# Optimization experiments

Hardware: AMD Instinct MI355X
Metric: run time of the kernel (lower is better)

## Reference

```python
import jax, jax.numpy as jnp
import numpy as np
from jax import lax

B, C1, C2, CM, H, W, K = 8, 256, 256, 128, 80, 80, 3
N = K * K
PAD = 1
EPS = 1e-5  # nn.BatchNorm2d default eps


def _bn(x, g, b, m, v):
    # eval-mode BatchNorm2d, NCHW
    inv = g / jnp.sqrt(v + EPS)
    return x * inv[None, :, None, None] + (b - m * inv)[None, :, None, None]


def _conv1x1(x, w):  # w: [O, I]
    return jnp.einsum('bihw,oi->bohw', x, w)


def _conv3x3(x, w, b):  # w: [O, I, 3, 3]
    y = lax.conv_general_dilated(x, w, window_strides=(1, 1),
                                 padding=((PAD, PAD), (PAD, PAD)),
                                 dimension_numbers=('NCHW', 'OIHW', 'NCHW'))
    return y + b[None, :, None, None]


def _deform_conv2d(x, offset, mask, w, bias):
    # DCNv2 (torchvision deform_conv2d semantics), stride=1, pad=1, k=3.
    # x: [B,C,H,W]; offset: [B,2N,H,W] pairs (dy,dx) per kernel tap (row-major);
    # mask: [B,N,H,W]; w: [O,C,3,3]
    Bx, C, Hx, Wx = x.shape
    ky, kx = jnp.meshgrid(jnp.arange(K), jnp.arange(K), indexing='ij')
    ky = ky.reshape(N).astype(x.dtype)
    kx = kx.reshape(N).astype(x.dtype)
    off = offset.reshape(Bx, N, 2, Hx, Wx)
    # sampling positions [B,N,H,W]
    py = (jnp.arange(Hx, dtype=x.dtype)[None, None, :, None] - PAD
          + ky[None, :, None, None] + off[:, :, 0])
    px = (jnp.arange(Wx, dtype=x.dtype)[None, None, None, :] - PAD
          + kx[None, :, None, None] + off[:, :, 1])

    y0 = jnp.floor(py)
    x0 = jnp.floor(px)
    wy1 = py - y0  # frac weights
    wx1 = px - x0
    x_flat = x.reshape(Bx, C, Hx * Wx)

    def corner(yi, xi, wgt):
        valid = (yi >= 0) & (yi < Hx) & (xi >= 0) & (xi < Wx)
        yc = jnp.clip(yi, 0, Hx - 1).astype(jnp.int32)
        xc = jnp.clip(xi, 0, Wx - 1).astype(jnp.int32)
        idx = (yc * Wx + xc).reshape(Bx, 1, N * Hx * Wx)
        g = jnp.take_along_axis(x_flat, idx, axis=2).reshape(Bx, C, N, Hx, Wx)
        return g * (wgt * valid.astype(x.dtype))[:, None]

    sampled = (corner(y0, x0, (1 - wy1) * (1 - wx1))
               + corner(y0, x0 + 1, (1 - wy1) * wx1)
               + corner(y0 + 1, x0, wy1 * (1 - wx1))
               + corner(y0 + 1, x0 + 1, wy1 * wx1))
    sampled = sampled * mask[:, None]  # modulated (v2)
    out = jnp.einsum('bcnhw,ocn->bohw', sampled, w.reshape(w.shape[0], C, N))
    return out + bias[None, :, None, None]


def setup_inputs() -> dict:
    key = jax.random.key(0)
    ks = jax.random.split(key, 20)
    f32 = jnp.float32
    d = {}
    d['x'] = jax.random.normal(ks[0], (B, C1, H, W), dtype=f32)
    # cv1: 1x1 conv (no bias) + BN
    d['cv1_w'] = jax.random.normal(ks[1], (CM, C1), dtype=f32) * (1.0 / np.sqrt(C1))
    d['bn1_g'] = jax.random.uniform(ks[2], (CM,), dtype=f32, minval=0.5, maxval=1.5)
    d['bn1_b'] = jax.random.normal(ks[3], (CM,), dtype=f32) * 0.1
    d['bn1_m'] = jax.random.normal(ks[4], (CM,), dtype=f32) * 0.1
    d['bn1_v'] = jax.random.uniform(ks[5], (CM,), dtype=f32, minval=0.5, maxval=1.5)
    # offset conv: predicts 3*N channels (2N offsets + N mask logits)
    d['off_w'] = jax.random.normal(ks[6], (3 * N, CM, K, K), dtype=f32) * 0.01
    d['off_b'] = jax.random.normal(ks[7], (3 * N,), dtype=f32) * 0.1
    # deformable conv main weight/bias
    d['dcn_w'] = jax.random.normal(ks[8], (CM, CM, K, K), dtype=f32) * np.sqrt(2.0 / (CM * N))
    d['dcn_b'] = jnp.zeros((CM,), dtype=f32)
    d['bn2_g'] = jax.random.uniform(ks[9], (CM,), dtype=f32, minval=0.5, maxval=1.5)
    d['bn2_b'] = jax.random.normal(ks[10], (CM,), dtype=f32) * 0.1
    d['bn2_m'] = jax.random.normal(ks[11], (CM,), dtype=f32) * 0.1
    d['bn2_v'] = jax.random.uniform(ks[12], (CM,), dtype=f32, minval=0.5, maxval=1.5)
    # cv3: 1x1 conv + BN
    d['cv3_w'] = jax.random.normal(ks[13], (C2, CM), dtype=f32) * (1.0 / np.sqrt(CM))
    d['bn3_g'] = jax.random.uniform(ks[14], (C2,), dtype=f32, minval=0.5, maxval=1.5)
    d['bn3_b'] = jax.random.normal(ks[15], (C2,), dtype=f32) * 0.1
    d['bn3_m'] = jax.random.normal(ks[16], (C2,), dtype=f32) * 0.1
    d['bn3_v'] = jax.random.uniform(ks[17], (C2,), dtype=f32, minval=0.5, maxval=1.5)
    return d


def reference(x, cv1_w, bn1_g, bn1_b, bn1_m, bn1_v,
              off_w, off_b, dcn_w, dcn_b,
              bn2_g, bn2_b, bn2_m, bn2_v,
              cv3_w, bn3_g, bn3_b, bn3_m, bn3_v):
    y = jax.nn.silu(_bn(_conv1x1(x, cv1_w), bn1_g, bn1_b, bn1_m, bn1_v))
    pred = _conv3x3(y, off_w, off_b)          # [B,3N,H,W]
    offset = pred[:, :2 * N]
    mask = jax.nn.sigmoid(pred[:, 2 * N:])
    y = _deform_conv2d(y, offset, mask, dcn_w, dcn_b)
    y = jax.nn.silu(_bn(y, bn2_g, bn2_b, bn2_m, bn2_v))
    y = jax.nn.silu(_bn(_conv1x1(y, cv3_w), bn3_g, bn3_b, bn3_m, bn3_v))
    return x + y  # shortcut: c1 == c2
```

## Files before the change

### kernel.cpp

```cpp
#include <hip/hip_runtime.h>
#include <math.h>

#define HWX   6400
#define WID   80
#define HGT   80
#define CMID  128
#define CIN   256
#define COUT  256

#define WS_PRED 0
#define WS_BN   1382400
#define WS_Y2   1383424
#define WS_Z2   4660224
#define WS_WPK  7937024
#define WS_WPO  8010752
#define WS_WP1  8029184
#define WS_WP3  8045568

typedef float floatx16 __attribute__((ext_vector_type(16)));
typedef short shortx8  __attribute__((ext_vector_type(8)));
typedef float floatx2  __attribute__((ext_vector_type(2)));

union U8 { uint32_t u[4]; shortx8 s; };

__device__ __forceinline__ float silu_f(float t){ return t / (1.f + __expf(-t)); }
__device__ __forceinline__ uint32_t f2bf(float f){
    uint32_t u = __float_as_uint(f);
    return (u + 0x7fffu + ((u >> 16) & 1u)) >> 16;
}
__device__ __forceinline__ floatx2 up2(uint32_t u){
    floatx2 r; r.x = __uint_as_float(u << 16); r.y = __uint_as_float(u & 0xffff0000u); return r;
}
__device__ __forceinline__ uint32_t pk2(floatx2 v){
    return __builtin_amdgcn_perm(__float_as_uint(v.y) + 0x8000u,
                                 __float_as_uint(v.x) + 0x8000u, 0x07060302u);
}
__device__ __forceinline__ uint32_t pk2f(float a, float b){ floatx2 v; v.x=a; v.y=b; return pk2(v); }

__global__ __launch_bounds__(256) void k0_prep(
    const float* __restrict__ dcn_w, const float* __restrict__ off_w,
    const float* __restrict__ cv1_w, const float* __restrict__ cv3_w,
    const float* __restrict__ g1, const float* __restrict__ b1, const float* __restrict__ m1, const float* __restrict__ v1,
    const float* __restrict__ g2, const float* __restrict__ b2, const float* __restrict__ m2, const float* __restrict__ v2,
    const float* __restrict__ dcn_b,
    const float* __restrict__ g3, const float* __restrict__ b3, const float* __restrict__ m3, const float* __restrict__ v3,
    uint32_t* __restrict__ wpk, uint32_t* __restrict__ wpo,
    uint32_t* __restrict__ wp1, uint32_t* __restrict__ wp3, float* __restrict__ bnw)
{
    int i = blockIdx.x * 256 + threadIdx.x;
    if (i < 4*9*8*256) {
        int j = i & 3, lane = (i >> 2) & 63, s = (i >> 8) & 7;
        int r2 = i >> 11; int tap = r2 % 9, g = r2 / 9;
        int oc = g*32 + (lane & 31);
        int c  = s*16 + ((lane >> 5) << 3) + 2*j;
        wpk[i] = f2bf(dcn_w[(oc*128 + c)*9 + tap]) | (f2bf(dcn_w[(oc*128 + c + 1)*9 + tap]) << 16);
    }
    if (i < 9*8*256) {
        int j = i & 3, lane = (i >> 2) & 63, s = (i >> 8) & 7, tap = i >> 11;
        int oc = lane & 31;
        int c  = s*16 + ((lane >> 5) << 3) + 2*j;
        float lo = (oc < 27) ? off_w[(oc*128 + c)*9 + tap] : 0.f;
        float hi = (oc < 27) ? off_w[(oc*128 + c + 1)*9 + tap] : 0.f;
        wpo[i] = f2bf(lo) | (f2bf(hi) << 16);
    }
    if (i < 4*16*256) {
        int j = i & 3, lane = (i >> 2) & 63, s = (i >> 8) & 15, g = i >> 12;
        int oc = g*32 + (lane & 31);
        int c  = s*16 + ((lane >> 5) << 3) + 2*j;
        wp1[i] = f2bf(cv1_w[oc*256 + c]) | (f2bf(cv1_w[oc*256 + c + 1]) << 16);
    }
    if (i < 8*8*256) {
        int j = i & 3, lane = (i >> 2) & 63, s = (i >> 8) & 7, g = i >> 11;
        int oc = g*32 + (lane & 31);
        int c  = s*16 + ((lane >> 5) << 3) + 2*j;
        wp3[i] = f2bf(cv3_w[oc*128 + c]) | (f2bf(cv3_w[oc*128 + c + 1]) << 16);
    }
    if (i < 128) {
        float inv = g1[i] * rsqrtf(v1[i] + 1e-5f);
        bnw[i] = inv; bnw[128+i] = b1[i] - m1[i]*inv;
    } else if (i < 256) {
        int j = i - 128;
        float inv = g2[j] * rsqrtf(v2[j] + 1e-5f);
        bnw[256+j] = inv; bnw[384+j] = b2[j] - m2[j]*inv + inv*dcn_b[j];
    } else if (i < 512) {
        int j = i - 256;
        float inv = g3[j] * rsqrtf(v3[j] + 1e-5f);
        bnw[512+j] = inv; bnw[768+j] = b3[j] - m3[j]*inv;
    }
}

#define K1PAD 68
__global__ __launch_bounds__(256) void k1_cv1(
    const float* __restrict__ x, const uint32_t* __restrict__ wp1,
    const float* __restrict__ bn, uint32_t* __restrict__ y2)
{
    __shared__ __align__(16) uint32_t L[64*66];
    int blk = blockIdx.x;
    int b = blk / 100, pix0 = (blk % 100) * 64;
    int t = threadIdx.x;
    int lane = t & 63, w = t >> 6;
    int pixl = lane & 31, bhalf = lane >> 5;
    floatx16 acc0 = {}, acc1 = {};
    const float* xb = x + (size_t)b*CIN*HWX + pix0;
    const uint32_t* wpg = wp1 + (size_t)(w*16)*256 + lane*4;

    int r2 = t >> 4, c4 = (t & 15) * 4;
    for (int kk = 0; kk < 256; kk += 32) {
        float4 a0 = *(const float4*)(xb + (size_t)(kk + 2*r2)*HWX + c4);
        float4 a1 = *(const float4*)(xb + (size_t)(kk + 2*r2 + 1)*HWX + c4);
        uint4 q;
        q.x = pk2f(a0.x, a1.x);
        q.y = pk2f(a0.y, a1.y);
        q.z = pk2f(a0.z, a1.z);
        q.w = pk2f(a0.w, a1.w);
        __syncthreads();
        *(uint4*)&L[r2*K1PAD + c4] = q;
        __syncthreads();
        #pragma unroll
        for (int sl = 0; sl < 2; sl++) {
            int s = (kk >> 4) + sl;
            U8 a, b0, b1;
            const uint32_t* as = wpg + s*256;
            a.u[0]=as[0]; a.u[1]=as[1]; a.u[2]=as[2]; a.u[3]=as[3];
            int row = sl*8 + bhalf*4;
            #pragma unroll
            for (int j = 0; j < 4; j++) b0.u[j] = L[(row+j)*K1PAD + pixl];
            #pragma unroll
            for (int j = 0; j < 4; j++) b1.u[j] = L[(row+j)*K1PAD + 32 + pixl];
            acc0 = __builtin_amdgcn_mfma_f32_32x32x16_bf16(a.s, b0.s, acc0, 0, 0, 0);
            acc1 = __builtin_amdgcn_mfma_f32_32x32x16_bf16(a.s, b1.s, acc1, 0, 0, 0);
        }
    }
    __syncthreads();
    #pragma unroll
    for (int r = 0; r < 16; r += 2) {
        int oc = w*32 + (r & 3) + 8*(r >> 2) + 4*bhalf;
        float s0 = bn[oc],   be0 = bn[128+oc];
        float s1 = bn[oc+1], be1 = bn[128+oc+1];
        uint32_t d0 = pk2f(silu_f(acc0[r]*s0+be0), silu_f(acc0[r+1]*s1+be1));
        uint32_t d1 = pk2f(silu_f(acc1[r]*s0+be0), silu_f(acc1[r+1]*s1+be1));
        int oc2 = oc >> 1;
        L[pixl*66 + oc2]        = d0;
        L[(32+pixl)*66 + oc2]   = d1;
    }
    __syncthreads();
    uint32_t* y2b = y2 + (size_t)b*HWX*64 + (size_t)pix0*64;
    int q2 = t & 31, p0 = t >> 5;
    #pragma unroll
    for (int pp = 0; pp < 8; pp++) {
        int pix = p0 + pp*8;
        uint2 v = make_uint2(L[pix*66 + q2*2], L[pix*66 + q2*2 + 1]);
        *(uint2*)(y2b + (size_t)pix*64 + q2*2) = v;
    }
}

__global__ __launch_bounds__(256) void k2_off(
    const uint32_t* __restrict__ y2, const uint32_t* __restrict__ wpo,
    const float* __restrict__ ob, float* __restrict__ pred)
{
    int blk = blockIdx.x;
    int b = blk / 50, pix0 = (blk % 50) * 128;
    int t = threadIdx.x;
    int lane = t & 63, w = t >> 6;
    int pixl = lane & 31, half = lane >> 5;
    int p = pix0 + w*32 + pixl;
    int h = p / WID, xw = p % WID;
    const uint32_t* yb = y2 + (size_t)b*HWX*64;
    floatx16 acc = {};

    for (int tap = 0; tap < 9; tap++) {
        int dy = tap/3 - 1, dx = tap%3 - 1;
        int gh = h + dy, gx = xw + dx;
        bool valid = (gh >= 0) && (gh < HGT) && (gx >= 0) && (gx < WID);
        const uint32_t* pp = yb + (size_t)(gh*WID + gx)*64 + half*4;
        const uint32_t* ap = wpo + (size_t)(tap*8)*256 + lane*4;
        #pragma unroll
        for (int s = 0; s < 8; s++) {
            U8 a, bf;
            const uint32_t* as = ap + s*256;
            a.u[0]=as[0]; a.u[1]=as[1]; a.u[2]=as[2]; a.u[3]=as[3];
            if (valid) {
                uint4 q = *(const uint4*)(pp + s*8);
                bf.u[0]=q.x; bf.u[1]=q.y; bf.u[2]=q.z; bf.u[3]=q.w;
            } else {
                bf.u[0]=0u; bf.u[1]=0u; bf.u[2]=0u; bf.u[3]=0u;
            }
            acc = __builtin_amdgcn_mfma_f32_32x32x16_bf16(a.s, bf.s, acc, 0, 0, 0);
        }
    }
    float* pb = pred + (size_t)b*27*HWX;
    #pragma unroll
    for (int r = 0; r < 16; r++) {
        int oc = (r & 3) + 8*(r >> 2) + 4*half;
        if (oc < 27) {
            float v = acc[r] + ob[oc];
            if (oc >= 18) v = 1.f/(1.f+__expf(-v));
            pb[oc*HWX + p] = v;
        }
    }
}

#define S2R 68
__global__ __launch_bounds__(256) void k3_dcn(
    const uint32_t* __restrict__ y2, const float* __restrict__ pred,
    const uint32_t* __restrict__ wpk, const float* __restrict__ bn, uint32_t* __restrict__ z2)
{
    __shared__ __align__(16) uint32_t S2[2][32*S2R];
    __shared__ __align__(16) int   sidx9[9*32*4];
    __shared__ __align__(16) float swgt9[9*32*4];
    int blk = blockIdx.x;
    int b = blk / 200, pix0 = (blk % 200) * 32;
    int t = threadIdx.x;
    int lane = t & 63, w = t >> 6;
    int pixl = lane & 31, bhalf = lane >> 5;
    const float* pb = pred + (size_t)b*27*HWX;
    const uint32_t* yb = y2 + (size_t)b*HWX*64;
    floatx16 acc = {};
    int c4 = lane & 31, pixoff = lane >> 5;

    for (int it = t; it < 288; it += 256) {
        int tap = it >> 5, px = it & 31;
        int pix = pix0 + px;
        int h = pix / WID, wq = pix % WID;
        float dy = pb[(2*tap)*HWX + pix];
        float dx = pb[(2*tap+1)*HWX + pix];
        float mk = pb[(18+tap)*HWX + pix];
        float pyf = (float)(h - 1 + tap/3) + dy;
        float pxf = (float)(wq - 1 + tap%3) + dx;
        float y0f = floorf(pyf), x0f = floorf(pxf);
        float wy1 = pyf - y0f, wx1 = pxf - x0f;
        int iy0 = (int)y0f, ix0 = (int)x0f;
        int iy1 = iy0 + 1,  ix1 = ix0 + 1;
        float vy0 = (iy0 >= 0 && iy0 < HGT) ? 1.f : 0.f;
        float vy1 = (iy1 >= 0 && iy1 < HGT) ? 1.f : 0.f;
        float vx0 = (ix0 >= 0 && ix0 < WID) ? 1.f : 0.f;
        float vx1 = (ix1 >= 0 && ix1 < WID) ? 1.f : 0.f;
        int cy0 = min(max(iy0,0),HGT-1), cy1 = min(max(iy1,0),HGT-1);
        int cx0 = min(max(ix0,0),WID-1), cx1 = min(max(ix1,0),WID-1);
        int base = (tap*32 + px)*4;
        sidx9[base+0] = cy0*WID+cx0; sidx9[base+1] = cy0*WID+cx1;
        sidx9[base+2] = cy1*WID+cx0; sidx9[base+3] = cy1*WID+cx1;
        swgt9[base+0] = (1.f-wy1)*(1.f-wx1)*mk*vy0*vx0;
        swgt9[base+1] = (1.f-wy1)*wx1*mk*vy0*vx1;
        swgt9[base+2] = wy1*(1.f-wx1)*mk*vy1*vx0;
        swgt9[base+3] = wy1*wx1*mk*vy1*vx1;
    }
    __syncthreads();

    uint2  u[4][4];
    float4 W[4];
    uint2  samp[4];

    #pragma unroll
    for (int p = 0; p < 4; p++) {
        int pix = w*8 + p*2 + pixoff;
        int base = (0*32 + pix)*4;
        int4 si = *(const int4*)&sidx9[base];
        W[p] = *(const float4*)&swgt9[base];
        u[p][0] = *(const uint2*)(yb + (size_t)si.x*64 + c4*2);
        u[p][1] = *(const uint2*)(yb + (size_t)si.y*64 + c4*2);
        u[p][2] = *(const uint2*)(yb + (size_t)si.z*64 + c4*2);
        u[p][3] = *(const uint2*)(yb + (size_t)si.w*64 + c4*2);
    }
    #pragma unroll
    for (int p = 0; p < 4; p++) {
        floatx2 W0, W1, W2, W3;
        W0.x = W0.y = W[p].x; W1.x = W1.y = W[p].y;
        W2.x = W2.y = W[p].z; W3.x = W3.y = W[p].w;
        floatx2 aX = up2(u[p][0].x) * W0;
        aX = __builtin_elementwise_fma(up2(u[p][1].x), W1, aX);
        aX = __builtin_elementwise_fma(up2(u[p][2].x), W2, aX);
        aX = __builtin_elementwise_fma(up2(u[p][3].x), W3, aX);
        floatx2 aY = up2(u[p][0].y) * W0;
        aY = __builtin_elementwise_fma(up2(u[p][1].y), W1, aY);
        aY = __builtin_elementwise_fma(up2(u[p][2].y), W2, aY);
        aY = __builtin_elementwise_fma(up2(u[p][3].y), W3, aY);
        samp[p].x = pk2(aX); samp[p].y = pk2(aY);
    }

    #pragma unroll
    for (int tap = 0; tap < 9; tap++) {
        uint32_t* S = &S2[tap & 1][0];
        #pragma unroll
        for (int p = 0; p < 4; p++) {
            int pix = w*8 + p*2 + pixoff;
            *(uint2*)&S[pix*S2R + c4*2] = samp[p];
        }
        __syncthreads();
        if (tap < 8) {
            #pragma unroll
            for (int p = 0; p < 4; p++) {
                int pix = w*8 + p*2 + pixoff;
                int base = ((tap+1)*32 + pix)*4;
                int4 si = *(const int4*)&sidx9[base];
                W[p] = *(const float4*)&swgt9[base];
                u[p][0] = *(const uint2*)(yb + (size_t)si.x*64 + c4*2);
                u[p][1] = *(const uint2*)(yb + (size_t)si.y*64 + c4*2);
                u[p][2] = *(const uint2*)(yb + (size_t)si.z*64 + c4*2);
                u[p][3] = *(const uint2*)(yb + (size_t)si.w*64 + c4*2);
            }
        }
        const uint32_t* wp = wpk + (size_t)((w*9 + tap)*8)*256 + lane*4;
        #pragma unroll
        for (int s = 0; s < 8; s++) {
            U8 a, bf;
            const uint32_t* wps = wp + s*256;
            a.u[0] = wps[0]; a.u[1] = wps[1]; a.u[2] = wps[2]; a.u[3] = wps[3];
            uint4 q = *(const uint4*)&S[pixl*S2R + s*8 + bhalf*4];
            bf.u[0]=q.x; bf.u[1]=q.y; bf.u[2]=q.z; bf.u[3]=q.w;
            acc = __builtin_amdgcn_mfma_f32_32x32x16_bf16(a.s, bf.s, acc, 0, 0, 0);
        }
        if (tap < 8) {
            #pragma unroll
            for (int p = 0; p < 4; p++) {
                floatx2 W0, W1, W2, W3;
                W0.x = W0.y = W[p].x; W1.x = W1.y = W[p].y;
                W2.x = W2.y = W[p].z; W3.x = W3.y = W[p].w;
                floatx2 aX = up2(u[p][0].x) * W0;
                aX = __builtin_elementwise_fma(up2(u[p][1].x), W1, aX);
                aX = __builtin_elementwise_fma(up2(u[p][2].x), W2, aX);
                aX = __builtin_elementwise_fma(up2(u[p][3].x), W3, aX);
                floatx2 aY = up2(u[p][0].y) * W0;
                aY = __builtin_elementwise_fma(up2(u[p][1].y), W1, aY);
                aY = __builtin_elementwise_fma(up2(u[p][2].y), W2, aY);
                aY = __builtin_elementwise_fma(up2(u[p][3].y), W3, aY);
                samp[p].x = pk2(aX); samp[p].y = pk2(aY);
            }
        }
    }
    uint32_t* SE = &S2[1][0];
    #pragma unroll
    for (int r = 0; r < 16; r += 2) {
        int oc = w*32 + (r & 3) + 8*(r >> 2) + 4*bhalf;
        float s0 = bn[256+oc],   be0 = bn[384+oc];
        float s1 = bn[256+oc+1], be1 = bn[384+oc+1];
        SE[pixl*S2R + (oc >> 1)] = pk2f(silu_f(acc[r]*s0+be0), silu_f(acc[r+1]*s1+be1));
    }
    __syncthreads();
    uint32_t* z2b = z2 + (size_t)b*HWX*64 + (size_t)pix0*64;
    int q2 = t & 31, p0 = t >> 5;
    #pragma unroll
    for (int pp = 0; pp < 4; pp++) {
        int pix = p0 + pp*8;
        uint2 v = *(const uint2*)&SE[pix*S2R + q2*2];
        *(uint2*)(z2b + (size_t)pix*64 + q2*2) = v;
    }
}

__global__ __launch_bounds__(256) void k4_cv3(
    const uint32_t* __restrict__ z2, const uint32_t* __restrict__ wp3,
    const float* __restrict__ bn, const float* __restrict__ x, float* __restrict__ out)
{
    int blk = blockIdx.x;
    int half = blk & 1, blk2 = blk >> 1;
    int b = blk2 / 100, pix0 = (blk2 % 100) * 64;
    int t = threadIdx.x;
    int lane = t & 63, w = t >> 6;
    int pixl = lane & 31, bhalf = lane >> 5;
    int g = half*4 + w;
    floatx16 acc0 = {}, acc1 = {};
    const uint32_t* zb = z2 + (size_t)b*HWX*64 + (size_t)pix0*64;
    const uint32_t* wpg = wp3 + (size_t)(g*8)*256 + lane*4;

    #pragma unroll
    for (int s = 0; s < 8; s++) {
        U8 a, b0, b1;
        const uint32_t* as = wpg + s*256;
        a.u[0]=as[0]; a.u[1]=as[1]; a.u[2]=as[2]; a.u[3]=as[3];
        uint4 q0 = *(const uint4*)(zb + (size_t)pixl*64 + s*8 + bhalf*4);
        uint4 q1 = *(const uint4*)(zb + (size_t)(32+pixl)*64 + s*8 + bhalf*4);
        b0.u[0]=q0.x; b0.u[1]=q0.y; b0.u[2]=q0.z; b0.u[3]=q0.w;
        b1.u[0]=q1.x; b1.u[1]=q1.y; b1.u[2]=q1.z; b1.u[3]=q1.w;
        acc0 = __builtin_amdgcn_mfma_f32_32x32x16_bf16(a.s, b0.s, acc0, 0, 0, 0);
        acc1 = __builtin_amdgcn_mfma_f32_32x32x16_bf16(a.s, b1.s, acc1, 0, 0, 0);
    }
    const float* xb = x + (size_t)b*COUT*HWX + pix0;
    float* ob = out + (size_t)b*COUT*HWX + pix0;
    #pragma unroll
    for (int r = 0; r < 16; r++) {
        int oc = g*32 + (r & 3) + 8*(r >> 2) + 4*bhalf;
        float sc = bn[512+oc], be = bn[768+oc];
        float v0 = silu_f(acc0[r]*sc+be) + xb[(size_t)oc*HWX + pixl];
        float v1 = silu_f(acc1[r]*sc+be) + xb[(size_t)oc*HWX + 32 + pixl];
        ob[(size_t)oc*HWX + pixl]      = v0;
        ob[(size_t)oc*HWX + 32 + pixl] = v1;
    }
}

extern "C" void kernel_launch(void* const* d_in, const int* in_sizes, int n_in,
                              void* d_out, int out_size, void* d_ws, size_t ws_size,
                              hipStream_t stream) {
    const float* x     = (const float*)d_in[0];
    const float* cv1_w = (const float*)d_in[1];
    const float* bn1_g = (const float*)d_in[2];
    const float* bn1_b = (const float*)d_in[3];
    const float* bn1_m = (const float*)d_in[4];
    const float* bn1_v = (const float*)d_in[5];
    const float* off_w = (const float*)d_in[6];
    const float* off_b = (const float*)d_in[7];
    const float* dcn_w = (const float*)d_in[8];
    const float* dcn_b = (const float*)d_in[9];
    const float* bn2_g = (const float*)d_in[10];
    const float* bn2_b = (const float*)d_in[11];
    const float* bn2_m = (const float*)d_in[12];
    const float* bn2_v = (const float*)d_in[13];
    const float* cv3_w = (const float*)d_in[14];
    const float* bn3_g = (const float*)d_in[15];
    const float* bn3_b = (const float*)d_in[16];
    const float* bn3_m = (const float*)d_in[17];
    const float* bn3_v = (const float*)d_in[18];

    float* ws   = (float*)d_ws;
    float*    PRED = ws + WS_PRED;
    float*    BN   = ws + WS_BN;
    uint32_t* Y2   = (uint32_t*)(ws + WS_Y2);
    uint32_t* Z2   = (uint32_t*)(ws + WS_Z2);
    uint32_t* WPK  = (uint32_t*)(ws + WS_WPK);
    uint32_t* WPO  = (uint32_t*)(ws + WS_WPO);
    uint32_t* WP1  = (uint32_t*)(ws + WS_WP1);
    uint32_t* WP3  = (uint32_t*)(ws + WS_WP3);

    hipLaunchKernelGGL(k0_prep, dim3(288), dim3(256), 0, stream,
        dcn_w, off_w, cv1_w, cv3_w,
        bn1_g, bn1_b, bn1_m, bn1_v,
        bn2_g, bn2_b, bn2_m, bn2_v, dcn_b,
        bn3_g, bn3_b, bn3_m, bn3_v, WPK, WPO, WP1, WP3, BN);
    hipLaunchKernelGGL(k1_cv1, dim3(800), dim3(256), 0, stream, x, WP1, BN, Y2);
    hipLaunchKernelGGL(k2_off, dim3(400), dim3(256), 0, stream, Y2, WPO, off_b, PRED);
    hipLaunchKernelGGL(k3_dcn, dim3(1600), dim3(256), 0, stream, Y2, PRED, WPK, BN, Z2);
    hipLaunchKernelGGL(k4_cv3, dim3(1600), dim3(256), 0, stream, Z2, WP3, BN, x, (float*)d_out);
}
```

Baseline: 238.6 us.

## Fuse offset/mask conv into deformable conv kernel, dropping pred buffer

Removes the separate offset-prediction kernel and computes the 3x3 offset/mask conv inside the DCN kernel for each 32-pixel tile. The taps are split across the 4 waves and the partial sums are reduced through shared memory reused from the S2 buffer. This avoids a kernel launch and the global write and read of the 27-channel pred tensor. In exchange it adds MFMA work and global neighbour loads to every DCN block, with only 32 pixels per tile, plus an extra shared-memory reduction and two barriers.

```diff
diff --git a/kernel.cpp b/kernel.cpp
--- a/kernel.cpp
+++ b/kernel.cpp
@@ -8,14 +8,13 @@
 #define CIN   256
 #define COUT  256
 
-#define WS_PRED 0
-#define WS_BN   1382400
-#define WS_Y2   1383424
-#define WS_Z2   4660224
-#define WS_WPK  7937024
-#define WS_WPO  8010752
-#define WS_WP1  8029184
-#define WS_WP3  8045568
+#define WS_BN   0
+#define WS_Y2   1024
+#define WS_Z2   3277824
+#define WS_WPK  6554624
+#define WS_WPO  6628352
+#define WS_WP1  6646784
+#define WS_WP3  6663168
 
 typedef float floatx16 __attribute__((ext_vector_type(16)));
 typedef short shortx8  __attribute__((ext_vector_type(8)));
@@ -154,55 +153,10 @@
     }
 }
 
-__global__ __launch_bounds__(256) void k2_off(
-    const uint32_t* __restrict__ y2, const uint32_t* __restrict__ wpo,
-    const float* __restrict__ ob, float* __restrict__ pred)
-{
-    int blk = blockIdx.x;
-    int b = blk / 50, pix0 = (blk % 50) * 128;
-    int t = threadIdx.x;
-    int lane = t & 63, w = t >> 6;
-    int pixl = lane & 31, half = lane >> 5;
-    int p = pix0 + w*32 + pixl;
-    int h = p / WID, xw = p % WID;
-    const uint32_t* yb = y2 + (size_t)b*HWX*64;
-    floatx16 acc = {};
-
-    for (int tap = 0; tap < 9; tap++) {
-        int dy = tap/3 - 1, dx = tap%3 - 1;
-        int gh = h + dy, gx = xw + dx;
-        bool valid = (gh >= 0) && (gh < HGT) && (gx >= 0) && (gx < WID);
-        const uint32_t* pp = yb + (size_t)(gh*WID + gx)*64 + half*4;
-        const uint32_t* ap = wpo + (size_t)(tap*8)*256 + lane*4;
-        #pragma unroll
-        for (int s = 0; s < 8; s++) {
-            U8 a, bf;
-            const uint32_t* as = ap + s*256;
-            a.u[0]=as[0]; a.u[1]=as[1]; a.u[2]=as[2]; a.u[3]=as[3];
-            if (valid) {
-                uint4 q = *(const uint4*)(pp + s*8);
-                bf.u[0]=q.x; bf.u[1]=q.y; bf.u[2]=q.z; bf.u[3]=q.w;
-            } else {
-                bf.u[0]=0u; bf.u[1]=0u; bf.u[2]=0u; bf.u[3]=0u;
-            }
-            acc = __builtin_amdgcn_mfma_f32_32x32x16_bf16(a.s, bf.s, acc, 0, 0, 0);
-        }
-    }
-    float* pb = pred + (size_t)b*27*HWX;
-    #pragma unroll
-    for (int r = 0; r < 16; r++) {
-        int oc = (r & 3) + 8*(r >> 2) + 4*half;
-        if (oc < 27) {
-            float v = acc[r] + ob[oc];
-            if (oc >= 18) v = 1.f/(1.f+__expf(-v));
-            pb[oc*HWX + p] = v;
-        }
-    }
-}
-
 #define S2R 68
 __global__ __launch_bounds__(256) void k3_dcn(
-    const uint32_t* __restrict__ y2, const float* __restrict__ pred,
+    const uint32_t* __restrict__ y2, const uint32_t* __restrict__ wpo,
+    const float* __restrict__ ob,
     const uint32_t* __restrict__ wpk, const float* __restrict__ bn, uint32_t* __restrict__ z2)
 {
     __shared__ __align__(16) uint32_t S2[2][32*S2R];
@@ -213,18 +167,64 @@
     int t = threadIdx.x;
     int lane = t & 63, w = t >> 6;
     int pixl = lane & 31, bhalf = lane >> 5;
-    const float* pb = pred + (size_t)b*27*HWX;
     const uint32_t* yb = y2 + (size_t)b*HWX*64;
     floatx16 acc = {};
     int c4 = lane & 31, pixoff = lane >> 5;
+    float* LF = (float*)&S2[0][0];
+
+    {
+        floatx16 accp = {};
+        int tap0 = (w < 3) ? w*2 : 6;
+        int ntap = (w < 3) ? 2 : 3;
+        int p = pix0 + pixl;
+        int h = p / WID, xw = p % WID;
+        for (int tt = 0; tt < ntap; tt++) {
+            int tap = tap0 + tt;
+            int gh = h + tap/3 - 1, gx = xw + tap%3 - 1;
+            bool valid = (gh >= 0) && (gh < HGT) && (gx >= 0) && (gx < WID);
+            const uint32_t* pp2 = yb + (size_t)(gh*WID + gx)*64 + bhalf*4;
+            const uint32_t* ap = wpo + (size_t)(tap*8)*256 + lane*4;
+            #pragma unroll
+            for (int s = 0; s < 8; s++) {
+                U8 a, bf;
+                const uint32_t* as = ap + s*256;
+                a.u[0]=as[0]; a.u[1]=as[1]; a.u[2]=as[2]; a.u[3]=as[3];
+                if (valid) {
+                    uint4 q = *(const uint4*)(pp2 + s*8);
+                    bf.u[0]=q.x; bf.u[1]=q.y; bf.u[2]=q.z; bf.u[3]=q.w;
+                } else {
+                    bf.u[0]=0u; bf.u[1]=0u; bf.u[2]=0u; bf.u[3]=0u;
+                }
+                accp = __builtin_amdgcn_mfma_f32_32x32x16_bf16(a.s, bf.s, accp, 0, 0, 0);
+            }
+        }
+        #pragma unroll
+        for (int r = 0; r < 16; r++) {
+            int oc = (r & 3) + 8*(r >> 2) + 4*bhalf;
+            LF[w*1024 + oc*32 + pixl] = accp[r];
+        }
+    }
+    __syncthreads();
+    #pragma unroll
+    for (int k = 0; k < 4; k++) {
+        int e = t + 256*k;
+        int oc = e >> 5;
+        float v = LF[e] + LF[1024+e] + LF[2048+e] + LF[3072+e];
+        if (oc < 27) {
+            v += ob[oc];
+            if (oc >= 18) v = 1.f/(1.f+__expf(-v));
+        }
+        LF[e] = v;
+    }
+    __syncthreads();
 
     for (int it = t; it < 288; it += 256) {
         int tap = it >> 5, px = it & 31;
         int pix = pix0 + px;
         int h = pix / WID, wq = pix % WID;
-        float dy = pb[(2*tap)*HWX + pix];
-        float dx = pb[(2*tap+1)*HWX + pix];
-        float mk = pb[(18+tap)*HWX + pix];
+        float dy = LF[(2*tap)*32 + px];
+        float dx = LF[(2*tap+1)*32 + px];
+        float mk = LF[(18+tap)*32 + px];
         float pyf = (float)(h - 1 + tap/3) + dy;
         float pxf = (float)(wq - 1 + tap%3) + dx;
         float y0f = floorf(pyf), x0f = floorf(pxf);
@@ -411,7 +411,6 @@
     const float* bn3_v = (const float*)d_in[18];
 
     float* ws   = (float*)d_ws;
-    float*    PRED = ws + WS_PRED;
     float*    BN   = ws + WS_BN;
     uint32_t* Y2   = (uint32_t*)(ws + WS_Y2);
     uint32_t* Z2   = (uint32_t*)(ws + WS_Z2);
@@ -426,7 +425,6 @@
         bn2_g, bn2_b, bn2_m, bn2_v, dcn_b,
         bn3_g, bn3_b, bn3_m, bn3_v, WPK, WPO, WP1, WP3, BN);
     hipLaunchKernelGGL(k1_cv1, dim3(800), dim3(256), 0, stream, x, WP1, BN, Y2);
-    hipLaunchKernelGGL(k2_off, dim3(400), dim3(256), 0, stream, Y2, WPO, off_b, PRED);
-    hipLaunchKernelGGL(k3_dcn, dim3(1600), dim3(256), 0, stream, Y2, PRED, WPK, BN, Z2);
+    hipLaunchKernelGGL(k3_dcn, dim3(1600), dim3(256), 0, stream, Y2, WPO, off_b, WPK, BN, Z2);
     hipLaunchKernelGGL(k4_cv3, dim3(1600), dim3(256), 0, stream, Z2, WP3, BN, x, (float*)d_out);
 }
```

Result: no change. 235.0 us (-1.5%).
